# Kernel optimization log

Measured on AMD Instinct MI355X. Metric: run time of the kernel, lower is better.

Reference implementation:

```python
import jax, jax.numpy as jnp
import numpy as np

NUM_HEADS = 16
HEAD_DIM = 64
CONTEXT = 128


def setup_inputs() -> dict:
    key = jax.random.key(0)
    k1, k2, k3, k4, k5 = jax.random.split(key, 5)
    B, S, H = 4, 4096, 1024
    inputs = jax.random.normal(k1, (B, S, H), dtype=jnp.float32)
    attention_mask = jnp.ones((B, S), dtype=jnp.int32)
    s = 1.0 / np.sqrt(H)
    Wq = jax.random.normal(k2, (H, H), dtype=jnp.float32) * s
    Wk = jax.random.normal(k3, (H, H), dtype=jnp.float32) * s
    Wv = jax.random.normal(k4, (H, H), dtype=jnp.float32) * s
    Wo = jax.random.normal(k5, (H, H), dtype=jnp.float32) * s
    return {"inputs": inputs, "attention_mask": attention_mask,
            "Wq": Wq, "Wk": Wk, "Wv": Wv, "Wo": Wo}


def reference(inputs, attention_mask, Wq, Wk, Wv, Wo):
    B, S, H = inputs.shape
    nH, dh = NUM_HEADS, HEAD_DIM
    C = min(CONTEXT, S)
    ctx_start = max(0, S - C)
    scale = 1.0 / np.sqrt(dh)

    # Q from all positions; K/V only from the recent context window
    q = (inputs @ Wq.T).reshape(B, S, nH, dh).transpose(0, 2, 1, 3)      # [B,nH,S,dh]
    ctx_in = inputs[:, ctx_start:, :]                                    # [B,C,H]
    k = (ctx_in @ Wk.T).reshape(B, C, nH, dh).transpose(0, 2, 1, 3)      # [B,nH,C,dh]
    v = (ctx_in @ Wv.T).reshape(B, C, nH, dh).transpose(0, 2, 1, 3)      # [B,nH,C,dh]

    scores = jnp.einsum('bhsd,bhcd->bhsc', q, k) * scale                 # [B,nH,S,C]

    # causal mask: context position <= query position; queries strictly
    # before the context window may attend to the first context token
    qpos = jnp.arange(S)
    cpos = jnp.arange(ctx_start, ctx_start + C)
    causal = cpos[None, :] <= qpos[:, None]                              # [S,C]
    before = qpos < ctx_start
    causal = causal.at[:, 0].set(causal[:, 0] | before)
    mask = causal[None, None, :, :]                                      # [1,1,S,C]

    # padding mask on context tokens
    ctx_pad = (attention_mask[:, ctx_start:ctx_start + C] != 0)          # [B,C]
    mask = mask & ctx_pad[:, None, None, :]

    scores = jnp.where(mask, scores, -jnp.inf)
    weights = jax.nn.softmax(scores, axis=-1)

    out = jnp.einsum('bhsc,bhcd->bhsd', weights, v)                      # [B,nH,S,dh]
    out = out.transpose(0, 2, 1, 3).reshape(B, S, H)
    return out @ Wo.T
```

## Files before the change

kernel.cpp:

```cpp
#include <hip/hip_runtime.h>
#include <math.h>

#define B_ 4
#define S_ 4096
#define H_ 1024
#define NH 16
#define DH 64
#define CTX 128
#define CSTART (S_ - CTX)
#define KDIM 1024

typedef __attribute__((ext_vector_type(8))) short short8;
typedef __attribute__((ext_vector_type(4))) float floatx4;
typedef unsigned short ushort_t;

__device__ inline unsigned short f2bf(float x) {
    union { float f; unsigned u; } v; v.f = x;
    unsigned r = v.u + 0x7fffu + ((v.u >> 16) & 1u);
    return (unsigned short)(r >> 16);
}

__device__ inline float bf2f(ushort_t u) {
    union { unsigned u; float f; } v; v.u = ((unsigned)u) << 16; return v.f;
}

__device__ inline uint4 pack8(float4 a, float4 b) {
    union { unsigned short us[8]; uint4 u4; } p;
    p.us[0]=f2bf(a.x); p.us[1]=f2bf(a.y); p.us[2]=f2bf(a.z); p.us[3]=f2bf(a.w);
    p.us[4]=f2bf(b.x); p.us[5]=f2bf(b.y); p.us[6]=f2bf(b.z); p.us[7]=f2bf(b.w);
    return p.u4;
}

__device__ inline float4 add4(float4 a, float4 b) {
    float4 r; r.x=a.x+b.x; r.y=a.y+b.y; r.z=a.z+b.z; r.w=a.w+b.w; return r;
}

#define GLOAD_LDS16(g, l) \
    __builtin_amdgcn_global_load_lds((__attribute__((address_space(1))) const void*)(g), \
                                     (__attribute__((address_space(3))) void*)(l), 16, 0, 0)

__global__ __launch_bounds__(256) void qkv_gemm(const float* __restrict__ in,
                                                const float* __restrict__ Wq,
                                                const float* __restrict__ Wk,
                                                const float* __restrict__ Wv,
                                                float* __restrict__ Pq) {
    __shared__ ushort_t As[64][64];
    __shared__ ushort_t Bs[64][64];
    int bid = blockIdx.x;
    int z = bid / 384;
    int rem = bid - z * 384;
    int x = rem % 48, y = rem / 48;
    int m0 = y * 64, n0 = x * 64, koff = z * 512;
    const float* Wsrc = (n0 < 1024) ? Wq : (n0 < 2048) ? Wk : Wv;
    int nrow0 = n0 & 1023;

    int tid = threadIdx.x;
    int lane = tid & 63, w = tid >> 6;
    int r0 = tid >> 3, g0 = (tid & 7) ^ (r0 & 7);
    int r1 = r0 + 32,  g1 = (tid & 7) ^ (r1 & 7);

    int am0 = m0 + r0, am1 = m0 + r1;
    const float* gaA0 = in + (size_t)((am0 >> 7) * S_ + CSTART + (am0 & 127)) * H_ + koff + g0 * 8;
    const float* gaA1 = in + (size_t)((am1 >> 7) * S_ + CSTART + (am1 & 127)) * H_ + koff + g1 * 8;
    const float* gaB0 = Wsrc + (size_t)(nrow0 + r0) * 1024 + koff + g0 * 8;
    const float* gaB1 = Wsrc + (size_t)(nrow0 + r1) * 1024 + koff + g1 * 8;
    uint4* lsA0 = (uint4*)((char*)As + tid * 16);
    uint4* lsA1 = (uint4*)((char*)As + tid * 16 + 4096);
    uint4* lsB0 = (uint4*)((char*)Bs + tid * 16);
    uint4* lsB1 = (uint4*)((char*)Bs + tid * 16 + 4096);

    int fm = lane & 15, q = lane >> 4;
    int wr = w >> 1, wc = w & 1;
    int ma0 = wr * 32, na0 = wc * 32;
    floatx4 acc[2][2] = {};

    float4 ra0, ra1, ra2, ra3, rb0, rb1, rb2, rb3;
#define LOAD_REGS_K1(k) do { \
        ra0 = *(const float4*)(gaA0 + (k));     ra1 = *(const float4*)(gaA0 + (k) + 4); \
        ra2 = *(const float4*)(gaA1 + (k));     ra3 = *(const float4*)(gaA1 + (k) + 4); \
        rb0 = *(const float4*)(gaB0 + (k));     rb1 = *(const float4*)(gaB0 + (k) + 4); \
        rb2 = *(const float4*)(gaB1 + (k));     rb3 = *(const float4*)(gaB1 + (k) + 4); } while (0)

    LOAD_REGS_K1(0);
    for (int k0 = 0; k0 < 512; k0 += 64) {
        uint4 pa0 = pack8(ra0, ra1), pa1 = pack8(ra2, ra3);
        uint4 pb0 = pack8(rb0, rb1), pb1 = pack8(rb2, rb3);
        if (k0) __syncthreads();
        *lsA0 = pa0; *lsA1 = pa1; *lsB0 = pb0; *lsB1 = pb1;
        __syncthreads();
        if (k0 + 64 < 512) LOAD_REGS_K1(k0 + 64);
        #pragma unroll
        for (int kb = 0; kb < 2; kb++) {
            short8 af[2], bfr[2];
            #pragma unroll
            for (int t = 0; t < 2; t++) {
                int m = ma0 + t * 16 + fm;
                int pa = (kb * 4 + q) ^ (m & 7);
                af[t] = *(const short8*)(&As[m][pa * 8]);
                int n = na0 + t * 16 + fm;
                int pb = (kb * 4 + q) ^ (n & 7);
                bfr[t] = *(const short8*)(&Bs[n][pb * 8]);
            }
            #pragma unroll
            for (int i = 0; i < 2; i++)
                #pragma unroll
                for (int j = 0; j < 2; j++)
                    acc[i][j] = __builtin_amdgcn_mfma_f32_16x16x32_bf16(af[i], bfr[j], acc[i][j], 0, 0, 0);
        }
    }
    float* outp = Pq + (size_t)z * 512 * 3072;
    #pragma unroll
    for (int i = 0; i < 2; i++)
        #pragma unroll
        for (int j = 0; j < 2; j++) {
            int row = m0 + ma0 + i * 16 + q * 4;
            int col = n0 + na0 + j * 16 + fm;
            #pragma unroll
            for (int t = 0; t < 4; t++)
                outp[(size_t)(row + t) * 3072 + col] = acc[i][j][t];
        }
}

__global__ __launch_bounds__(256) void attn(const float* __restrict__ Pq,
                                            const int* __restrict__ amask,
                                            ushort_t* __restrict__ AO) {
    __shared__ __align__(16) char smem[46080];
    ushort_t* Qs   = (ushort_t*)(smem);
    ushort_t* Ksh  = (ushort_t*)(smem + 9216);
    ushort_t* Pb   = (ushort_t*)(smem);
    float*    linv = (float*)(smem + 27648);
    int*      amk  = (int*)(smem + 27904);
    ushort_t* Vt   = (ushort_t*)(smem + 28416);

    int gid = blockIdx.x;
    int b = gid >> 5, h = (gid >> 1) & 15, half = gid & 1;
    int tid = threadIdx.x;
    int cmax = half ? CTX : 64;
    {
        int r = tid >> 2, ch = tid & 3;
        size_t qb = (size_t)(b * CTX + half * 64 + r) * 3072 + h * 64 + ch * 16;
        const float4* q0 = (const float4*)(Pq + qb);
        const float4* q1 = (const float4*)(Pq + (size_t)512 * 3072 + qb);
        float4 a0 = add4(q0[0], q1[0]), a1 = add4(q0[1], q1[1]);
        float4 a2 = add4(q0[2], q1[2]), a3 = add4(q0[3], q1[3]);
        *(uint4*)(Qs + r * 72 + ch * 16)     = pack8(a0, a1);
        *(uint4*)(Qs + r * 72 + ch * 16 + 8) = pack8(a2, a3);
        for (int idx = tid; idx < cmax * 4; idx += 256) {
            int kr = idx >> 2, kch = idx & 3;
            size_t base = (size_t)(b * CTX + kr) * 3072 + h * 64 + kch * 16;
            const float4* p0 = (const float4*)(Pq + base);
            const float4* p1 = (const float4*)(Pq + (size_t)512 * 3072 + base);
            float4 k0 = add4(p0[256], p1[256]), k1 = add4(p0[257], p1[257]);
            float4 k2 = add4(p0[258], p1[258]), k3 = add4(p0[259], p1[259]);
            *(uint4*)(Ksh + kr * 72 + kch * 16)     = pack8(k0, k1);
            *(uint4*)(Ksh + kr * 72 + kch * 16 + 8) = pack8(k2, k3);
            float vv[16];
            #pragma unroll
            for (int c4 = 0; c4 < 4; c4++) {
                float4 s = add4(p0[512 + c4], p1[512 + c4]);
                vv[c4*4+0]=s.x; vv[c4*4+1]=s.y; vv[c4*4+2]=s.z; vv[c4*4+3]=s.w;
            }
            #pragma unroll
            for (int i = 0; i < 16; i++)
                Vt[(kch * 16 + i) * 136 + kr] = f2bf(vv[i]);
        }
        if (tid < 128) amk[tid] = amask[b * S_ + CSTART + tid];
    }
    __syncthreads();

    int w = tid >> 6, lane = tid & 63;
    int qt = half * 4 + w;
    int lr0 = w * 16;
    int fm = lane & 15, quad = lane >> 4;

    short8 af[2];
    #pragma unroll
    for (int kb = 0; kb < 2; kb++)
        af[kb] = *(const short8*)(Qs + (lr0 + fm) * 72 + kb * 32 + quad * 8);
    floatx4 acc[8] = {};
    for (int ct = 0; ct <= qt; ct++) {
        #pragma unroll
        for (int kb = 0; kb < 2; kb++) {
            short8 bfr = *(const short8*)(Ksh + (ct * 16 + fm) * 72 + kb * 32 + quad * 8);
            acc[ct] = __builtin_amdgcn_mfma_f32_16x16x32_bf16(af[kb], bfr, acc[ct], 0, 0, 0);
        }
    }
    int myamk[8];
    #pragma unroll
    for (int ct = 0; ct < 8; ct++) myamk[ct] = amk[ct * 16 + fm];
    float ls[4];
    #pragma unroll
    for (int t = 0; t < 4; t++) {
        int row = qt * 16 + quad * 4 + t;
        float m = -INFINITY;
        #pragma unroll
        for (int ct = 0; ct < 8; ct++) {
            int col = ct * 16 + fm;
            float s = acc[ct][t] * 0.125f;
            bool valid = (ct <= qt) && (col <= row) && (myamk[ct] != 0);
            if (valid) m = fmaxf(m, s);
        }
        #pragma unroll
        for (int off = 8; off >= 1; off >>= 1) m = fmaxf(m, __shfl_xor(m, off, 64));
        float l = 0.f;
        #pragma unroll
        for (int ct = 0; ct < 8; ct++) {
            int col = ct * 16 + fm;
            float s = acc[ct][t] * 0.125f;
            bool valid = (ct <= qt) && (col <= row) && (myamk[ct] != 0);
            float p = valid ? __expf(s - m) : 0.f;
            acc[ct][t] = p;
            l += p;
        }
        #pragma unroll
        for (int off = 8; off >= 1; off >>= 1) l += __shfl_xor(l, off, 64);
        ls[t] = l;
    }
    __syncthreads();
    #pragma unroll
    for (int t = 0; t < 4; t++) {
        int lrow = lr0 + quad * 4 + t;
        #pragma unroll
        for (int ct = 0; ct < 8; ct++)
            Pb[lrow * 136 + ct * 16 + fm] = f2bf(acc[ct][t]);
        if (fm == 0) linv[lrow] = 1.f / ls[t];
    }
    int kmax = (qt >> 1) + 1;
    floatx4 oacc[4] = {};
    for (int kb = 0; kb < kmax; kb++) {
        short8 paf = *(const short8*)(Pb + (lr0 + fm) * 136 + kb * 32 + quad * 8);
        #pragma unroll
        for (int dt = 0; dt < 4; dt++) {
            short8 vbf = *(const short8*)(Vt + (dt * 16 + fm) * 136 + kb * 32 + quad * 8);
            oacc[dt] = __builtin_amdgcn_mfma_f32_16x16x32_bf16(paf, vbf, oacc[dt], 0, 0, 0);
        }
    }
    #pragma unroll
    for (int t = 0; t < 4; t++) {
        int lrow = lr0 + quad * 4 + t;
        int grow = qt * 16 + quad * 4 + t;
        float inv = linv[lrow];
        #pragma unroll
        for (int dt = 0; dt < 4; dt++)
            AO[(size_t)(b * CTX + grow) * H_ + h * 64 + dt * 16 + fm] = f2bf(oacc[dt][t] * inv);
    }
}

__global__ __launch_bounds__(256) void ogemm_bcast(const ushort_t* __restrict__ AObf,
                                                   const float* __restrict__ Wo,
                                                   float* __restrict__ out) {
    __shared__ __align__(16) char smem[16384];
    int bid = blockIdx.x;
    int tid = threadIdx.x;

    if (bid < 128) {
        ushort_t (*As)[64] = (ushort_t(*)[64])smem;
        ushort_t (*Bs)[64] = (ushort_t(*)[64])(smem + 8192);
        int x = bid % 16, y = bid / 16;
        int m0 = y * 64, n0 = x * 64;
        int lane = tid & 63, w = tid >> 6;
        int r0 = tid >> 3, g0 = (tid & 7) ^ (r0 & 7);
        int r1 = r0 + 32,  g1 = (tid & 7) ^ (r1 & 7);
        const ushort_t* ga0 = AObf + (size_t)(m0 + r0) * KDIM + g0 * 8;
        const ushort_t* ga1 = AObf + (size_t)(m0 + r1) * KDIM + g1 * 8;
        const float*    gb0 = Wo + (size_t)(n0 + r0) * 1024 + g0 * 8;
        const float*    gb1 = Wo + (size_t)(n0 + r1) * 1024 + g1 * 8;
        char* laA0 = smem + tid * 16;
        char* laA1 = smem + tid * 16 + 4096;
        uint4* lsB0 = (uint4*)(smem + 8192 + tid * 16);
        uint4* lsB1 = (uint4*)(smem + 8192 + tid * 16 + 4096);

        int fm = lane & 15, q = lane >> 4;
        int wr = w >> 1, wc = w & 1;
        int ma0 = wr * 32, na0 = wc * 32;
        floatx4 acc[2][2] = {};

        float4 rb0, rb1, rb2, rb3;
#define LOAD_REGS_K3(k) do { \
            rb0 = *(const float4*)(gb0 + (k)); rb1 = *(const float4*)(gb0 + (k) + 4); \
            rb2 = *(const float4*)(gb1 + (k)); rb3 = *(const float4*)(gb1 + (k) + 4); } while (0)

        LOAD_REGS_K3(0);
        for (int k0 = 0; k0 < 1024; k0 += 64) {
            uint4 pb0 = pack8(rb0, rb1), pb1 = pack8(rb2, rb3);
            if (k0) __syncthreads();
            GLOAD_LDS16(ga0 + k0, laA0);
            GLOAD_LDS16(ga1 + k0, laA1);
            *lsB0 = pb0; *lsB1 = pb1;
            __syncthreads();
            if (k0 + 64 < 1024) LOAD_REGS_K3(k0 + 64);
            #pragma unroll
            for (int kb = 0; kb < 2; kb++) {
                short8 af[2], bfr[2];
                #pragma unroll
                for (int t = 0; t < 2; t++) {
                    int m = ma0 + t * 16 + fm;
                    int pa = (kb * 4 + q) ^ (m & 7);
                    af[t] = *(const short8*)(&As[m][pa * 8]);
                    int n = na0 + t * 16 + fm;
                    int pb = (kb * 4 + q) ^ (n & 7);
                    bfr[t] = *(const short8*)(&Bs[n][pb * 8]);
                }
                #pragma unroll
                for (int i = 0; i < 2; i++)
                    #pragma unroll
                    for (int j = 0; j < 2; j++)
                        acc[i][j] = __builtin_amdgcn_mfma_f32_16x16x32_bf16(af[i], bfr[j], acc[i][j], 0, 0, 0);
            }
        }
        #pragma unroll
        for (int i = 0; i < 2; i++)
            #pragma unroll
            for (int j = 0; j < 2; j++) {
                int row = m0 + ma0 + i * 16 + q * 4;
                int col = n0 + na0 + j * 16 + fm;
                #pragma unroll
                for (int t = 0; t < 4; t++) {
                    int rr = row + t;
                    size_t gr = (size_t)((rr >> 7) * S_ + CSTART + (rr & 127));
                    out[gr * 1024 + col] = acc[i][j][t];
                }
            }
    } else {
        float* vals = (float*)smem;
        int idx = bid - 128;
        int c  = idx & 15;
        int b2 = (idx >> 4) & 3;
        int rc = idx >> 6;
        int n0 = c * 64;
        int w = tid >> 6, lane = tid & 63;
        int rsub = lane >> 4, kl = lane & 15;
        const ushort_t* ao = AObf + (size_t)(b2 * 128) * 1024;
        #pragma unroll
        for (int p = 0; p < 4; p++) {
            int rl = p * 16 + w * 4 + rsub;
            const float* wrow = Wo + (size_t)(n0 + rl) * 1024;
            float4 av = {0.f, 0.f, 0.f, 0.f};
            #pragma unroll
            for (int it = 0; it < 16; it++) {
                int k = kl * 4 + it * 64;
                float4 wv = *(const float4*)(wrow + k);
                av.x += wv.x * bf2f(ao[k]);
                av.y += wv.y * bf2f(ao[k + 1]);
                av.z += wv.z * bf2f(ao[k + 2]);
                av.w += wv.w * bf2f(ao[k + 3]);
            }
            float s = av.x + av.y + av.z + av.w;
            #pragma unroll
            for (int off = 1; off < 16; off <<= 1) s += __shfl_xor(s, off, 64);
            if (kl == 0) vals[rl] = s;
        }
        __syncthreads();
        int c4 = tid & 15, ro = tid >> 4;
        float4 v4 = *(const float4*)(vals + c4 * 4);
        size_t gbase = (size_t)b2 * S_ * 1024 + n0 + c4 * 4;
        #pragma unroll
        for (int i = 0; i < 31; i++) {
            int p = rc * 496 + ro + i * 16;
            *(float4*)(out + gbase + (size_t)p * 1024) = v4;
        }
    }
}

extern "C" void kernel_launch(void* const* d_in, const int* in_sizes, int n_in,
                              void* d_out, int out_size, void* d_ws, size_t ws_size,
                              hipStream_t stream) {
    const float* inputs = (const float*)d_in[0];
    const int*   amask  = (const int*)d_in[1];
    const float* Wq     = (const float*)d_in[2];
    const float* Wk     = (const float*)d_in[3];
    const float* Wv     = (const float*)d_in[4];
    const float* Wo     = (const float*)d_in[5];
    float* out = (float*)d_out;

    char* ws = (char*)d_ws;
    float*    Pq   = (float*)(ws);
    ushort_t* AObf = (ushort_t*)(ws + (13u << 20));

    qkv_gemm<<<768, 256, 0, stream>>>(inputs, Wq, Wk, Wv, Pq);
    attn<<<128, 256, 0, stream>>>(Pq, amask, AObf);
    ogemm_bcast<<<640, 256, 0, stream>>>(AObf, Wo, out);
}
```

Measured before the change: 155.8 us.

## Fuse QKV projection into attention kernel, one block per batch-head-half

Merges the split-K QKV GEMM and the attention kernel into a single kernel. Each of 128 blocks computes its head's Q, K and V projections for the 128 context rows over the full K=1024 and writes them straight into shared memory as bf16. This removes the fp32 partial-sum round trip through global memory and one kernel launch. In exchange, grid parallelism drops from 768 GEMM blocks to 128, K/V projections are computed twice (once per half), and the block needs large LDS and many accumulator registers.

```diff
diff --git a/kernel.cpp b/kernel.cpp
--- a/kernel.cpp
+++ b/kernel.cpp
@@ -31,158 +31,141 @@
     return p.u4;
 }
 
-__device__ inline float4 add4(float4 a, float4 b) {
-    float4 r; r.x=a.x+b.x; r.y=a.y+b.y; r.z=a.z+b.z; r.w=a.w+b.w; return r;
-}
-
 #define GLOAD_LDS16(g, l) \
     __builtin_amdgcn_global_load_lds((__attribute__((address_space(1))) const void*)(g), \
                                      (__attribute__((address_space(3))) void*)(l), 16, 0, 0)
 
-__global__ __launch_bounds__(256) void qkv_gemm(const float* __restrict__ in,
-                                                const float* __restrict__ Wq,
-                                                const float* __restrict__ Wk,
-                                                const float* __restrict__ Wv,
-                                                float* __restrict__ Pq) {
-    __shared__ ushort_t As[64][64];
-    __shared__ ushort_t Bs[64][64];
-    int bid = blockIdx.x;
-    int z = bid / 384;
-    int rem = bid - z * 384;
-    int x = rem % 48, y = rem / 48;
-    int m0 = y * 64, n0 = x * 64, koff = z * 512;
-    const float* Wsrc = (n0 < 1024) ? Wq : (n0 < 2048) ? Wk : Wv;
-    int nrow0 = n0 & 1023;
-
-    int tid = threadIdx.x;
+__global__ __launch_bounds__(256, 1) void qkva(const float* __restrict__ in,
+                                               const int* __restrict__ amask,
+                                               const float* __restrict__ Wq,
+                                               const float* __restrict__ Wk,
+                                               const float* __restrict__ Wv,
+                                               ushort_t* __restrict__ AO) {
+    __shared__ __align__(16) char smem[87040];
+    ushort_t* As = (ushort_t*)smem;
+    ushort_t* Bs = (ushort_t*)(smem + 16384);
+    char* ar = smem + 40960;
+    ushort_t* Qs   = (ushort_t*)(ar);
+    ushort_t* Ksh  = (ushort_t*)(ar + 9216);
+    ushort_t* Pb   = (ushort_t*)(ar);
+    float*    linv = (float*)(ar + 27648);
+    int*      amk  = (int*)(ar + 27904);
+    ushort_t* Vt   = (ushort_t*)(ar + 28416);
+
+    int bid = blockIdx.x, tid = threadIdx.x;
+    int b = bid >> 5, h = (bid >> 1) & 15, half = bid & 1;
     int lane = tid & 63, w = tid >> 6;
-    int r0 = tid >> 3, g0 = (tid & 7) ^ (r0 & 7);
-    int r1 = r0 + 32,  g1 = (tid & 7) ^ (r1 & 7);
-
-    int am0 = m0 + r0, am1 = m0 + r1;
-    const float* gaA0 = in + (size_t)((am0 >> 7) * S_ + CSTART + (am0 & 127)) * H_ + koff + g0 * 8;
-    const float* gaA1 = in + (size_t)((am1 >> 7) * S_ + CSTART + (am1 & 127)) * H_ + koff + g1 * 8;
-    const float* gaB0 = Wsrc + (size_t)(nrow0 + r0) * 1024 + koff + g0 * 8;
-    const float* gaB1 = Wsrc + (size_t)(nrow0 + r1) * 1024 + koff + g1 * 8;
-    uint4* lsA0 = (uint4*)((char*)As + tid * 16);
-    uint4* lsA1 = (uint4*)((char*)As + tid * 16 + 4096);
-    uint4* lsB0 = (uint4*)((char*)Bs + tid * 16);
-    uint4* lsB1 = (uint4*)((char*)Bs + tid * 16 + 4096);
-
     int fm = lane & 15, q = lane >> 4;
-    int wr = w >> 1, wc = w & 1;
-    int ma0 = wr * 32, na0 = wc * 32;
-    floatx4 acc[2][2] = {};
-
-    float4 ra0, ra1, ra2, ra3, rb0, rb1, rb2, rb3;
-#define LOAD_REGS_K1(k) do { \
-        ra0 = *(const float4*)(gaA0 + (k));     ra1 = *(const float4*)(gaA0 + (k) + 4); \
-        ra2 = *(const float4*)(gaA1 + (k));     ra3 = *(const float4*)(gaA1 + (k) + 4); \
-        rb0 = *(const float4*)(gaB0 + (k));     rb1 = *(const float4*)(gaB0 + (k) + 4); \
-        rb2 = *(const float4*)(gaB1 + (k));     rb3 = *(const float4*)(gaB1 + (k) + 4); } while (0)
-
-    LOAD_REGS_K1(0);
-    for (int k0 = 0; k0 < 512; k0 += 64) {
-        uint4 pa0 = pack8(ra0, ra1), pa1 = pack8(ra2, ra3);
-        uint4 pb0 = pack8(rb0, rb1), pb1 = pack8(rb2, rb3);
+
+    if (tid < 128) amk[tid] = amask[b * S_ + CSTART + tid];
+
+    int rA = tid >> 1, cA0 = (tid & 1) * 4, sA = rA & 7;
+    int rB = tid >> 2, cB0 = (tid & 3) * 2, sB = rB & 7;
+    const float* gA  = in + ((size_t)b * S_ + CSTART + rA) * H_ + cA0 * 8;
+    const float* gBq = Wq + (size_t)(h * 64 + rB) * 1024 + cB0 * 8;
+    const float* gBk = Wk + (size_t)(h * 64 + rB) * 1024 + cB0 * 8;
+    const float* gBv = Wv + (size_t)(h * 64 + rB) * 1024 + cB0 * 8;
+    ushort_t* wA = As + rA * 64;
+    ushort_t* wB = Bs + rB * 64;
+
+    floatx4 acc[2][12] = {};
+    float4 la[8], lb[12];
+#define LOADALL(k) do { \
+        _Pragma("unroll") \
+        for (int cc = 0; cc < 4; cc++) { \
+            la[2*cc]   = *(const float4*)(gA + (k) + cc * 8); \
+            la[2*cc+1] = *(const float4*)(gA + (k) + cc * 8 + 4); \
+        } \
+        _Pragma("unroll") \
+        for (int cc = 0; cc < 2; cc++) { \
+            lb[2*cc]     = *(const float4*)(gBq + (k) + cc * 8); \
+            lb[2*cc+1]   = *(const float4*)(gBq + (k) + cc * 8 + 4); \
+            lb[4+2*cc]   = *(const float4*)(gBk + (k) + cc * 8); \
+            lb[4+2*cc+1] = *(const float4*)(gBk + (k) + cc * 8 + 4); \
+            lb[8+2*cc]   = *(const float4*)(gBv + (k) + cc * 8); \
+            lb[8+2*cc+1] = *(const float4*)(gBv + (k) + cc * 8 + 4); \
+        } } while (0)
+
+    LOADALL(0);
+    for (int k0 = 0; k0 < 1024; k0 += 64) {
+        uint4 pa[4], pb[6];
+        #pragma unroll
+        for (int cc = 0; cc < 4; cc++) pa[cc] = pack8(la[2*cc], la[2*cc+1]);
+        #pragma unroll
+        for (int m = 0; m < 3; m++)
+            #pragma unroll
+            for (int cc = 0; cc < 2; cc++)
+                pb[m*2+cc] = pack8(lb[m*4+2*cc], lb[m*4+2*cc+1]);
         if (k0) __syncthreads();
-        *lsA0 = pa0; *lsA1 = pa1; *lsB0 = pb0; *lsB1 = pb1;
+        #pragma unroll
+        for (int cc = 0; cc < 4; cc++)
+            *(uint4*)(wA + ((cA0 + cc) ^ sA) * 8) = pa[cc];
+        #pragma unroll
+        for (int m = 0; m < 3; m++)
+            #pragma unroll
+            for (int cc = 0; cc < 2; cc++)
+                *(uint4*)(wB + m * 4096 + ((cB0 + cc) ^ sB) * 8) = pb[m*2+cc];
         __syncthreads();
-        if (k0 + 64 < 512) LOAD_REGS_K1(k0 + 64);
+        if (k0 + 64 < 1024) LOADALL(k0 + 64);
         #pragma unroll
         for (int kb = 0; kb < 2; kb++) {
-            short8 af[2], bfr[2];
-            #pragma unroll
-            for (int t = 0; t < 2; t++) {
-                int m = ma0 + t * 16 + fm;
-                int pa = (kb * 4 + q) ^ (m & 7);
-                af[t] = *(const short8*)(&As[m][pa * 8]);
-                int n = na0 + t * 16 + fm;
-                int pb = (kb * 4 + q) ^ (n & 7);
-                bfr[t] = *(const short8*)(&Bs[n][pb * 8]);
-            }
-            #pragma unroll
-            for (int i = 0; i < 2; i++)
+            short8 af[2];
+            #pragma unroll
+            for (int i = 0; i < 2; i++) {
+                int m = w * 32 + i * 16 + fm;
+                af[i] = *(const short8*)(As + m * 64 + (((kb * 4 + q) ^ (m & 7)) * 8));
+            }
+            #pragma unroll
+            for (int j = 0; j < 12; j++) {
+                int n = j * 16 + fm;
+                short8 bfr = *(const short8*)(Bs + n * 64 + (((kb * 4 + q) ^ (n & 7)) * 8));
+                acc[0][j] = __builtin_amdgcn_mfma_f32_16x16x32_bf16(af[0], bfr, acc[0][j], 0, 0, 0);
+                acc[1][j] = __builtin_amdgcn_mfma_f32_16x16x32_bf16(af[1], bfr, acc[1][j], 0, 0, 0);
+            }
+        }
+    }
+#undef LOADALL
+
+    bool qown = ((w >> 1) == half);
+    #pragma unroll
+    for (int i = 0; i < 2; i++) {
+        int rbase = w * 32 + i * 16 + q * 4;
+        if (qown) {
+            #pragma unroll
+            for (int j = 0; j < 4; j++)
                 #pragma unroll
-                for (int j = 0; j < 2; j++)
-                    acc[i][j] = __builtin_amdgcn_mfma_f32_16x16x32_bf16(af[i], bfr[j], acc[i][j], 0, 0, 0);
-        }
-    }
-    float* outp = Pq + (size_t)z * 512 * 3072;
-    #pragma unroll
-    for (int i = 0; i < 2; i++)
-        #pragma unroll
-        for (int j = 0; j < 2; j++) {
-            int row = m0 + ma0 + i * 16 + q * 4;
-            int col = n0 + na0 + j * 16 + fm;
+                for (int t = 0; t < 4; t++)
+                    Qs[((rbase & 63) + t) * 72 + j * 16 + fm] = f2bf(acc[i][j][t]);
+        }
+        #pragma unroll
+        for (int j = 4; j < 8; j++)
             #pragma unroll
             for (int t = 0; t < 4; t++)
-                outp[(size_t)(row + t) * 3072 + col] = acc[i][j][t];
-        }
-}
-
-__global__ __launch_bounds__(256) void attn(const float* __restrict__ Pq,
-                                            const int* __restrict__ amask,
-                                            ushort_t* __restrict__ AO) {
-    __shared__ __align__(16) char smem[46080];
-    ushort_t* Qs   = (ushort_t*)(smem);
-    ushort_t* Ksh  = (ushort_t*)(smem + 9216);
-    ushort_t* Pb   = (ushort_t*)(smem);
-    float*    linv = (float*)(smem + 27648);
-    int*      amk  = (int*)(smem + 27904);
-    ushort_t* Vt   = (ushort_t*)(smem + 28416);
-
-    int gid = blockIdx.x;
-    int b = gid >> 5, h = (gid >> 1) & 15, half = gid & 1;
-    int tid = threadIdx.x;
-    int cmax = half ? CTX : 64;
-    {
-        int r = tid >> 2, ch = tid & 3;
-        size_t qb = (size_t)(b * CTX + half * 64 + r) * 3072 + h * 64 + ch * 16;
-        const float4* q0 = (const float4*)(Pq + qb);
-        const float4* q1 = (const float4*)(Pq + (size_t)512 * 3072 + qb);
-        float4 a0 = add4(q0[0], q1[0]), a1 = add4(q0[1], q1[1]);
-        float4 a2 = add4(q0[2], q1[2]), a3 = add4(q0[3], q1[3]);
-        *(uint4*)(Qs + r * 72 + ch * 16)     = pack8(a0, a1);
-        *(uint4*)(Qs + r * 72 + ch * 16 + 8) = pack8(a2, a3);
-        for (int idx = tid; idx < cmax * 4; idx += 256) {
-            int kr = idx >> 2, kch = idx & 3;
-            size_t base = (size_t)(b * CTX + kr) * 3072 + h * 64 + kch * 16;
-            const float4* p0 = (const float4*)(Pq + base);
-            const float4* p1 = (const float4*)(Pq + (size_t)512 * 3072 + base);
-            float4 k0 = add4(p0[256], p1[256]), k1 = add4(p0[257], p1[257]);
-            float4 k2 = add4(p0[258], p1[258]), k3 = add4(p0[259], p1[259]);
-            *(uint4*)(Ksh + kr * 72 + kch * 16)     = pack8(k0, k1);
-            *(uint4*)(Ksh + kr * 72 + kch * 16 + 8) = pack8(k2, k3);
-            float vv[16];
-            #pragma unroll
-            for (int c4 = 0; c4 < 4; c4++) {
-                float4 s = add4(p0[512 + c4], p1[512 + c4]);
-                vv[c4*4+0]=s.x; vv[c4*4+1]=s.y; vv[c4*4+2]=s.z; vv[c4*4+3]=s.w;
-            }
-            #pragma unroll
-            for (int i = 0; i < 16; i++)
-                Vt[(kch * 16 + i) * 136 + kr] = f2bf(vv[i]);
-        }
-        if (tid < 128) amk[tid] = amask[b * S_ + CSTART + tid];
+                Ksh[(rbase + t) * 72 + (j - 4) * 16 + fm] = f2bf(acc[i][j][t]);
+        #pragma unroll
+        for (int j = 8; j < 12; j++) {
+            union { unsigned short us[4]; uint2 u2; } pk;
+            #pragma unroll
+            for (int t = 0; t < 4; t++) pk.us[t] = f2bf(acc[i][j][t]);
+            *(uint2*)(Vt + ((j - 8) * 16 + fm) * 136 + rbase) = pk.u2;
+        }
     }
     __syncthreads();
 
-    int w = tid >> 6, lane = tid & 63;
     int qt = half * 4 + w;
     int lr0 = w * 16;
-    int fm = lane & 15, quad = lane >> 4;
-
-    short8 af[2];
+    int quad = q;
+
+    short8 afq[2];
     #pragma unroll
     for (int kb = 0; kb < 2; kb++)
-        af[kb] = *(const short8*)(Qs + (lr0 + fm) * 72 + kb * 32 + quad * 8);
-    floatx4 acc[8] = {};
+        afq[kb] = *(const short8*)(Qs + (lr0 + fm) * 72 + kb * 32 + quad * 8);
+    floatx4 sc[8] = {};
     for (int ct = 0; ct <= qt; ct++) {
         #pragma unroll
         for (int kb = 0; kb < 2; kb++) {
             short8 bfr = *(const short8*)(Ksh + (ct * 16 + fm) * 72 + kb * 32 + quad * 8);
-            acc[ct] = __builtin_amdgcn_mfma_f32_16x16x32_bf16(af[kb], bfr, acc[ct], 0, 0, 0);
+            sc[ct] = __builtin_amdgcn_mfma_f32_16x16x32_bf16(afq[kb], bfr, sc[ct], 0, 0, 0);
         }
     }
     int myamk[8];
@@ -196,7 +179,7 @@
         #pragma unroll
         for (int ct = 0; ct < 8; ct++) {
             int col = ct * 16 + fm;
-            float s = acc[ct][t] * 0.125f;
+            float s = sc[ct][t] * 0.125f;
             bool valid = (ct <= qt) && (col <= row) && (myamk[ct] != 0);
             if (valid) m = fmaxf(m, s);
         }
@@ -206,10 +189,10 @@
         #pragma unroll
         for (int ct = 0; ct < 8; ct++) {
             int col = ct * 16 + fm;
-            float s = acc[ct][t] * 0.125f;
+            float s = sc[ct][t] * 0.125f;
             bool valid = (ct <= qt) && (col <= row) && (myamk[ct] != 0);
             float p = valid ? __expf(s - m) : 0.f;
-            acc[ct][t] = p;
+            sc[ct][t] = p;
             l += p;
         }
         #pragma unroll
@@ -222,7 +205,7 @@
         int lrow = lr0 + quad * 4 + t;
         #pragma unroll
         for (int ct = 0; ct < 8; ct++)
-            Pb[lrow * 136 + ct * 16 + fm] = f2bf(acc[ct][t]);
+            Pb[lrow * 136 + ct * 16 + fm] = f2bf(sc[ct][t]);
         if (fm == 0) linv[lrow] = 1.f / ls[t];
     }
     int kmax = (qt >> 1) + 1;
@@ -308,6 +291,7 @@
                         acc[i][j] = __builtin_amdgcn_mfma_f32_16x16x32_bf16(af[i], bfr[j], acc[i][j], 0, 0, 0);
             }
         }
+#undef LOAD_REGS_K3
         #pragma unroll
         for (int i = 0; i < 2; i++)
             #pragma unroll
@@ -373,11 +357,8 @@
     const float* Wo     = (const float*)d_in[5];
     float* out = (float*)d_out;
 
-    char* ws = (char*)d_ws;
-    float*    Pq   = (float*)(ws);
-    ushort_t* AObf = (ushort_t*)(ws + (13u << 20));
-
-    qkv_gemm<<<768, 256, 0, stream>>>(inputs, Wq, Wk, Wv, Pq);
-    attn<<<128, 256, 0, stream>>>(Pq, amask, AObf);
+    ushort_t* AObf = (ushort_t*)d_ws;
+
+    qkva<<<128, 256, 0, stream>>>(inputs, amask, Wq, Wk, Wv, AObf);
     ogemm_bcast<<<640, 256, 0, stream>>>(AObf, Wo, out);
 }
```

Measured after the change: 183.9 us. 1.18x slower.

## Drop split-K in QKV GEMM and store projections as bf16

Applied to the files above, without the earlier changes.

The QKV projection GEMM no longer splits K across two block groups. It now runs 384 blocks over the full K=1024 and writes a single bf16 result instead of two fp32 partial sums. The attention kernel loads Q/K/V directly as bf16, so it skips the partial-sum adds and fp32-to-bf16 conversion. This cuts workspace traffic and attention prologue work, but halves GEMM parallelism (384 blocks on 256 CUs) and doubles each block's K loop.

```diff
diff --git a/kernel.cpp b/kernel.cpp
--- a/kernel.cpp
+++ b/kernel.cpp
@@ -31,10 +31,6 @@
     return p.u4;
 }
 
-__device__ inline float4 add4(float4 a, float4 b) {
-    float4 r; r.x=a.x+b.x; r.y=a.y+b.y; r.z=a.z+b.z; r.w=a.w+b.w; return r;
-}
-
 #define GLOAD_LDS16(g, l) \
     __builtin_amdgcn_global_load_lds((__attribute__((address_space(1))) const void*)(g), \
                                      (__attribute__((address_space(3))) void*)(l), 16, 0, 0)
@@ -43,14 +39,12 @@
                                                 const float* __restrict__ Wq,
                                                 const float* __restrict__ Wk,
                                                 const float* __restrict__ Wv,
-                                                float* __restrict__ Pq) {
+                                                ushort_t* __restrict__ Pqb) {
     __shared__ ushort_t As[64][64];
     __shared__ ushort_t Bs[64][64];
     int bid = blockIdx.x;
-    int z = bid / 384;
-    int rem = bid - z * 384;
-    int x = rem % 48, y = rem / 48;
-    int m0 = y * 64, n0 = x * 64, koff = z * 512;
+    int x = bid % 48, y = bid / 48;
+    int m0 = y * 64, n0 = x * 64;
     const float* Wsrc = (n0 < 1024) ? Wq : (n0 < 2048) ? Wk : Wv;
     int nrow0 = n0 & 1023;
 
@@ -60,10 +54,10 @@
     int r1 = r0 + 32,  g1 = (tid & 7) ^ (r1 & 7);
 
     int am0 = m0 + r0, am1 = m0 + r1;
-    const float* gaA0 = in + (size_t)((am0 >> 7) * S_ + CSTART + (am0 & 127)) * H_ + koff + g0 * 8;
-    const float* gaA1 = in + (size_t)((am1 >> 7) * S_ + CSTART + (am1 & 127)) * H_ + koff + g1 * 8;
-    const float* gaB0 = Wsrc + (size_t)(nrow0 + r0) * 1024 + koff + g0 * 8;
-    const float* gaB1 = Wsrc + (size_t)(nrow0 + r1) * 1024 + koff + g1 * 8;
+    const float* gaA0 = in + (size_t)((am0 >> 7) * S_ + CSTART + (am0 & 127)) * H_ + g0 * 8;
+    const float* gaA1 = in + (size_t)((am1 >> 7) * S_ + CSTART + (am1 & 127)) * H_ + g1 * 8;
+    const float* gaB0 = Wsrc + (size_t)(nrow0 + r0) * 1024 + g0 * 8;
+    const float* gaB1 = Wsrc + (size_t)(nrow0 + r1) * 1024 + g1 * 8;
     uint4* lsA0 = (uint4*)((char*)As + tid * 16);
     uint4* lsA1 = (uint4*)((char*)As + tid * 16 + 4096);
     uint4* lsB0 = (uint4*)((char*)Bs + tid * 16);
@@ -82,13 +76,13 @@
         rb2 = *(const float4*)(gaB1 + (k));     rb3 = *(const float4*)(gaB1 + (k) + 4); } while (0)
 
     LOAD_REGS_K1(0);
-    for (int k0 = 0; k0 < 512; k0 += 64) {
+    for (int k0 = 0; k0 < 1024; k0 += 64) {
         uint4 pa0 = pack8(ra0, ra1), pa1 = pack8(ra2, ra3);
         uint4 pb0 = pack8(rb0, rb1), pb1 = pack8(rb2, rb3);
         if (k0) __syncthreads();
         *lsA0 = pa0; *lsA1 = pa1; *lsB0 = pb0; *lsB1 = pb1;
         __syncthreads();
-        if (k0 + 64 < 512) LOAD_REGS_K1(k0 + 64);
+        if (k0 + 64 < 1024) LOAD_REGS_K1(k0 + 64);
         #pragma unroll
         for (int kb = 0; kb < 2; kb++) {
             short8 af[2], bfr[2];
@@ -108,7 +102,7 @@
                     acc[i][j] = __builtin_amdgcn_mfma_f32_16x16x32_bf16(af[i], bfr[j], acc[i][j], 0, 0, 0);
         }
     }
-    float* outp = Pq + (size_t)z * 512 * 3072;
+#undef LOAD_REGS_K1
     #pragma unroll
     for (int i = 0; i < 2; i++)
         #pragma unroll
@@ -117,11 +111,11 @@
             int col = n0 + na0 + j * 16 + fm;
             #pragma unroll
             for (int t = 0; t < 4; t++)
-                outp[(size_t)(row + t) * 3072 + col] = acc[i][j][t];
-        }
-}
-
-__global__ __launch_bounds__(256) void attn(const float* __restrict__ Pq,
+                Pqb[(size_t)(row + t) * 3072 + col] = f2bf(acc[i][j][t]);
+        }
+}
+
+__global__ __launch_bounds__(256) void attn(const ushort_t* __restrict__ Pqb,
                                             const int* __restrict__ amask,
                                             ushort_t* __restrict__ AO) {
     __shared__ __align__(16) char smem[46080];
@@ -137,32 +131,22 @@
     int tid = threadIdx.x;
     int cmax = half ? CTX : 64;
     {
-        int r = tid >> 2, ch = tid & 3;
-        size_t qb = (size_t)(b * CTX + half * 64 + r) * 3072 + h * 64 + ch * 16;
-        const float4* q0 = (const float4*)(Pq + qb);
-        const float4* q1 = (const float4*)(Pq + (size_t)512 * 3072 + qb);
-        float4 a0 = add4(q0[0], q1[0]), a1 = add4(q0[1], q1[1]);
-        float4 a2 = add4(q0[2], q1[2]), a3 = add4(q0[3], q1[3]);
-        *(uint4*)(Qs + r * 72 + ch * 16)     = pack8(a0, a1);
-        *(uint4*)(Qs + r * 72 + ch * 16 + 8) = pack8(a2, a3);
+        int r = tid >> 2, c0 = (tid & 3) * 16;
+        const ushort_t* qsrc = Pqb + (size_t)(b * CTX + half * 64 + r) * 3072 + h * 64 + c0;
+        *(uint4*)(Qs + r * 72 + c0)     = *(const uint4*)(qsrc);
+        *(uint4*)(Qs + r * 72 + c0 + 8) = *(const uint4*)(qsrc + 8);
         for (int idx = tid; idx < cmax * 4; idx += 256) {
             int kr = idx >> 2, kch = idx & 3;
-            size_t base = (size_t)(b * CTX + kr) * 3072 + h * 64 + kch * 16;
-            const float4* p0 = (const float4*)(Pq + base);
-            const float4* p1 = (const float4*)(Pq + (size_t)512 * 3072 + base);
-            float4 k0 = add4(p0[256], p1[256]), k1 = add4(p0[257], p1[257]);
-            float4 k2 = add4(p0[258], p1[258]), k3 = add4(p0[259], p1[259]);
-            *(uint4*)(Ksh + kr * 72 + kch * 16)     = pack8(k0, k1);
-            *(uint4*)(Ksh + kr * 72 + kch * 16 + 8) = pack8(k2, k3);
-            float vv[16];
-            #pragma unroll
-            for (int c4 = 0; c4 < 4; c4++) {
-                float4 s = add4(p0[512 + c4], p1[512 + c4]);
-                vv[c4*4+0]=s.x; vv[c4*4+1]=s.y; vv[c4*4+2]=s.z; vv[c4*4+3]=s.w;
-            }
+            const ushort_t* kb = Pqb + (size_t)(b * CTX + kr) * 3072 + 1024 + h * 64 + kch * 16;
+            *(uint4*)(Ksh + kr * 72 + kch * 16)     = *(const uint4*)(kb);
+            *(uint4*)(Ksh + kr * 72 + kch * 16 + 8) = *(const uint4*)(kb + 8);
+            const ushort_t* vb = Pqb + (size_t)(b * CTX + kr) * 3072 + 2048 + h * 64 + kch * 16;
+            union { uint4 u[2]; ushort_t us[16]; } vv;
+            vv.u[0] = *(const uint4*)(vb);
+            vv.u[1] = *(const uint4*)(vb + 8);
             #pragma unroll
             for (int i = 0; i < 16; i++)
-                Vt[(kch * 16 + i) * 136 + kr] = f2bf(vv[i]);
+                Vt[(kch * 16 + i) * 136 + kr] = vv.us[i];
         }
         if (tid < 128) amk[tid] = amask[b * S_ + CSTART + tid];
     }
@@ -308,6 +292,7 @@
                         acc[i][j] = __builtin_amdgcn_mfma_f32_16x16x32_bf16(af[i], bfr[j], acc[i][j], 0, 0, 0);
             }
         }
+#undef LOAD_REGS_K3
         #pragma unroll
         for (int i = 0; i < 2; i++)
             #pragma unroll
@@ -374,10 +359,10 @@
     float* out = (float*)d_out;
 
     char* ws = (char*)d_ws;
-    float*    Pq   = (float*)(ws);
-    ushort_t* AObf = (ushort_t*)(ws + (13u << 20));
-
-    qkv_gemm<<<768, 256, 0, stream>>>(inputs, Wq, Wk, Wv, Pq);
-    attn<<<128, 256, 0, stream>>>(Pq, amask, AObf);
+    ushort_t* Pqb  = (ushort_t*)(ws);
+    ushort_t* AObf = (ushort_t*)(ws + (4u << 20));
+
+    qkv_gemm<<<384, 256, 0, stream>>>(inputs, Wq, Wk, Wv, Pqb);
+    attn<<<128, 256, 0, stream>>>(Pqb, amask, AObf);
     ogemm_bcast<<<640, 256, 0, stream>>>(AObf, Wo, out);
 }
```

After: 156.9 us. About the same (+0.7%).
